# Optimization experiments

Measured on AMD Instinct MI355X. Metric: run time of the kernel, lower is better.

Reference implementation:

```python
import jax, jax.numpy as jnp
import numpy as np

N, E, P, IN, H = 1024, 65536, 1024, 128, 64
LN_EPS = 1e-5


def _layernorm(x, g, b):
    mu = x.mean(-1, keepdims=True)
    var = ((x - mu) ** 2).mean(-1, keepdims=True)
    return (x - mu) * jax.lax.rsqrt(var + LN_EPS) * g + b


def _gcn(x, ei, W, b, n):
    # PyG GCNConv: out = D^{-1/2} (A + I) D^{-1/2} X W + b
    row, col = ei[0], ei[1]
    xw = x @ W
    deg = jnp.zeros((n,), xw.dtype).at[col].add(1.0) + 1.0  # self-loop adds 1
    dinv = jax.lax.rsqrt(deg)
    coef = (dinv[row] * dinv[col])[:, None]
    out = jnp.zeros_like(xw).at[col].add(xw[row] * coef)
    out = out + xw * (dinv * dinv)[:, None]  # self-loop message
    return out + b


def setup_inputs() -> dict:
    key = jax.random.key(0)
    ks = jax.random.split(key, 20)
    f32 = jnp.float32
    inp = {
        "x": jax.random.normal(ks[0], (N, IN), f32),
        "ei": jax.random.randint(ks[1], (2, E), 0, N, dtype=jnp.int32),
        "pos": jax.random.randint(ks[2], (2, P), 0, N, dtype=jnp.int32),
        # GCNConv(input, hidden) and GCNConv(hidden, hidden)
        "W_g1": jax.random.normal(ks[3], (IN, H), f32) * (IN ** -0.5),
        "b_g1": jnp.zeros((H,), f32),
        "W_g2": jax.random.normal(ks[4], (H, H), f32) * (H ** -0.5),
        "b_g2": jnp.zeros((H,), f32),
        # mlp1: Linear + LayerNorm (+Dropout eval=id) + ReLU
        "W_m1": jax.random.normal(ks[5], (H, H), f32) * (H ** -0.5),
        "b_m1": jnp.zeros((H,), f32),
        "g_m1": jnp.ones((H,), f32),
        "be_m1": jnp.zeros((H,), f32),
        # mlp2
        "W_m2": jax.random.normal(ks[6], (H, H), f32) * (H ** -0.5),
        "b_m2": jnp.zeros((H,), f32),
        "g_m2": jnp.ones((H,), f32),
        "be_m2": jnp.zeros((H,), f32),
        # mlp3: Linear(2H,H) + ReLU + Linear(H,1)
        "W_a": jax.random.normal(ks[7], (2 * H, H), f32) * ((2 * H) ** -0.5),
        "b_a": jnp.zeros((H,), f32),
        "W_b": jax.random.normal(ks[8], (H, 1), f32) * (H ** -0.5),
        "b_b": jnp.zeros((1,), f32),
    }
    return inp


def reference(x, ei, pos, W_g1, b_g1, W_g2, b_g2, W_m1, b_m1, g_m1, be_m1,
              W_m2, b_m2, g_m2, be_m2, W_a, b_a, W_b, b_b):
    n = x.shape[0]
    # forward_routine
    h = _gcn(x, ei, W_g1, b_g1, n)
    h = _gcn(h, ei, W_g2, b_g2, n)
    xx = h[pos[0]] * h[pos[1]]          # [P, H] pairwise node products at queries
    xe = h[ei[0]] * h[ei[1]]            # [E, H] pairwise node products at edges
    x1 = jax.nn.relu(_layernorm(xe @ W_m1 + b_m1, g_m1, be_m1))  # mlp1
    x2 = jax.nn.relu(_layernorm(xe @ W_m2 + b_m2, g_m2, be_m2))  # mlp2
    # dense_bmm / sparse_bmm followed by combine() keeps only entries at pos
    # pairs, so compute res[pos0, pos1, :] = sum_k D1[pos0, k, :] * D2[k, pos1, :]
    D1 = jnp.zeros((n, n, H), x2.dtype).at[ei[0], ei[1]].set(x2)  # mlp2 output: left operand
    D2 = jnp.zeros((n, n, H), x1.dtype).at[ei[0], ei[1]].set(x1)  # mlp1 output: right operand
    r1 = D1[pos[0]]                                   # [P, N, H]
    c2 = jnp.swapaxes(jnp.take(D2, pos[1], axis=1), 0, 1)  # [P, N, H]
    pos_val = jnp.einsum('pnh,pnh->ph', r1, c2)       # [P, H]
    feat = jnp.concatenate([pos_val, xx], axis=1)     # combine -> [P, 2H]
    hid = jax.nn.relu(feat @ W_a + b_a)               # mlp3 (dropout = identity at eval)
    return (hid @ W_b + b_b).squeeze(-1)              # [P]
```

## Files before the change

kernel.cpp:

```cpp
#include <hip/hip_runtime.h>

#define Nn 1024
#define Ee 65536
#define Pq 1024
#define CAP 160

typedef unsigned long long ull;

__global__ __launch_bounds__(256) void k_zero(uint4* __restrict__ z) {
    z[blockIdx.x * 256 + threadIdx.x] = make_uint4(0, 0, 0, 0);
}

__global__ __launch_bounds__(256) void k_front(const float* __restrict__ x,
                                               const float* __restrict__ Wg1,
                                               float* __restrict__ xw1,
                                               const int* __restrict__ ei,
                                               int* __restrict__ degI,
                                               int* __restrict__ adj,
                                               ull* __restrict__ Mbit,
                                               ull* __restrict__ MTbit) {
    __shared__ float sW[8192];
    int tid = threadIdx.x;
    int B = blockIdx.x;
    if (B < 256) {
        int gid = B * 256 + tid;
        for (int i = tid; i < 2048; i += 256)
            ((float4*)sW)[i] = ((const float4*)Wg1)[i];
        __syncthreads();
        int lane = gid & 63;
        int r = __builtin_amdgcn_readfirstlane(gid >> 6);
        const float* xr = x + r * 128;
        float acc = 0.f;
        #pragma unroll 8
        for (int j = 0; j < 128; ++j) acc = fmaf(xr[j], sW[j * 64 + lane], acc);
        xw1[gid] = acc;
    } else {
        int e = (B - 256) * 256 + tid;
        int r = ei[e], c = ei[Ee + e];
        int slot = atomicAdd(&degI[c], 1);
        if (slot < CAP) adj[c * CAP + slot] = r;
        atomicOr(&Mbit[r * 16 + (c >> 6)], 1ull << (c & 63));
        atomicOr(&MTbit[c * 16 + (r >> 6)], 1ull << (r & 63));
    }
}

__device__ __forceinline__ float gather_quarter(const int* __restrict__ s_adj,
                                                const float* __restrict__ xwsrc,
                                                const float* s_dinv, int w,
                                                int n, int lane) {
    float acc = 0.f;
    int j = w, end = n;
    for (; j + 28 < end; j += 32) {
        int r0 = s_adj[j],      r1 = s_adj[j + 4],  r2 = s_adj[j + 8],  r3 = s_adj[j + 12];
        int r4 = s_adj[j + 16], r5 = s_adj[j + 20], r6 = s_adj[j + 24], r7 = s_adj[j + 28];
        float a0 = xwsrc[r0 * 64 + lane] * s_dinv[r0];
        float a1 = xwsrc[r1 * 64 + lane] * s_dinv[r1];
        float a2 = xwsrc[r2 * 64 + lane] * s_dinv[r2];
        float a3 = xwsrc[r3 * 64 + lane] * s_dinv[r3];
        float a4 = xwsrc[r4 * 64 + lane] * s_dinv[r4];
        float a5 = xwsrc[r5 * 64 + lane] * s_dinv[r5];
        float a6 = xwsrc[r6 * 64 + lane] * s_dinv[r6];
        float a7 = xwsrc[r7 * 64 + lane] * s_dinv[r7];
        acc += ((a0 + a1) + (a2 + a3)) + ((a4 + a5) + (a6 + a7));
    }
    for (; j < end; j += 4) {
        int r = s_adj[j];
        acc += xwsrc[r * 64 + lane] * s_dinv[r];
    }
    return acc;
}

__global__ __launch_bounds__(256) void k_gather1(const int* __restrict__ adj,
                                                 const int* __restrict__ degI,
                                                 const float* __restrict__ xw1,
                                                 const float* __restrict__ Wg2,
                                                 const float* __restrict__ bg1,
                                                 float* __restrict__ xw2) {
    __shared__ float sW[4096];
    __shared__ float s_dinv[Nn];
    __shared__ int s_adj[CAP];
    __shared__ float red[4][64];
    int tid = threadIdx.x;
    int lane = tid & 63;
    int w = tid >> 6;
    int c = blockIdx.x;
    for (int i = tid; i < 1024; i += 256)
        ((float4*)sW)[i] = ((const float4*)Wg2)[i];
    {
        int4 d4 = ((const int4*)degI)[tid];
        s_dinv[4 * tid]     = rsqrtf((float)d4.x + 1.f);
        s_dinv[4 * tid + 1] = rsqrtf((float)d4.y + 1.f);
        s_dinv[4 * tid + 2] = rsqrtf((float)d4.z + 1.f);
        s_dinv[4 * tid + 3] = rsqrtf((float)d4.w + 1.f);
    }
    int n = __builtin_amdgcn_readfirstlane(degI[c]);
    if (n > CAP) n = CAP;
    if (tid < n) s_adj[tid] = adj[c * CAP + tid];
    __syncthreads();
    float acc = gather_quarter(s_adj, xw1, s_dinv, w, n, lane);
    red[w][lane] = acc;
    __syncthreads();
    if (w == 0) {
        float a = (red[0][lane] + red[1][lane]) + (red[2][lane] + red[3][lane]);
        float dc = s_dinv[c];
        float h1c = dc * a + dc * dc * xw1[c * 64 + lane] + bg1[lane];
        float t = 0.f;
        #pragma unroll 8
        for (int j = 0; j < 64; ++j) t = fmaf(__shfl(h1c, j), sW[j * 64 + lane], t);
        xw2[c * 64 + lane] = t;
    }
}

__global__ __launch_bounds__(256) void k_gather2(const int* __restrict__ adj,
                                                 const int* __restrict__ degI,
                                                 const float* __restrict__ xw2,
                                                 const float* __restrict__ bg2,
                                                 float* __restrict__ h2) {
    __shared__ float s_dinv[Nn];
    __shared__ int s_adj[CAP];
    __shared__ float red[4][64];
    int tid = threadIdx.x;
    int lane = tid & 63;
    int w = tid >> 6;
    int c = blockIdx.x;
    {
        int4 d4 = ((const int4*)degI)[tid];
        s_dinv[4 * tid]     = rsqrtf((float)d4.x + 1.f);
        s_dinv[4 * tid + 1] = rsqrtf((float)d4.y + 1.f);
        s_dinv[4 * tid + 2] = rsqrtf((float)d4.z + 1.f);
        s_dinv[4 * tid + 3] = rsqrtf((float)d4.w + 1.f);
    }
    int n = __builtin_amdgcn_readfirstlane(degI[c]);
    if (n > CAP) n = CAP;
    if (tid < n) s_adj[tid] = adj[c * CAP + tid];
    __syncthreads();
    float acc = gather_quarter(s_adj, xw2, s_dinv, w, n, lane);
    red[w][lane] = acc;
    __syncthreads();
    if (w == 0) {
        float a = (red[0][lane] + red[1][lane]) + (red[2][lane] + red[3][lane]);
        float dc = s_dinv[c];
        h2[c * 64 + lane] = dc * a + dc * dc * xw2[c * 64 + lane] + bg2[lane];
    }
}

__global__ __launch_bounds__(256) void k_posfinal(
    const int* __restrict__ pos,
    const ull* __restrict__ Mbit, const ull* __restrict__ MTbit,
    const float* __restrict__ h2,
    const float* __restrict__ W1, const float* __restrict__ b1,
    const float* __restrict__ g1, const float* __restrict__ be1,
    const float* __restrict__ W2, const float* __restrict__ b2,
    const float* __restrict__ g2, const float* __restrict__ be2,
    const float* __restrict__ Wa, const float* __restrict__ ba,
    const float* __restrict__ Wb, const float* __restrict__ bb,
    float* __restrict__ out) {
    __shared__ float W1s[4096], W2s[4096];
    __shared__ float s_red[3][64];
    int tid = threadIdx.x;
    for (int i = tid; i < 1024; i += 256) {
        ((float4*)W1s)[i] = ((const float4*)W1)[i];
        ((float4*)W2s)[i] = ((const float4*)W2)[i];
    }
    __syncthreads();
    int lane = tid & 63;
    int wv = tid >> 6;
    int p = blockIdx.x;
    int a = __builtin_amdgcn_readfirstlane(pos[p]);
    int b = __builtin_amdgcn_readfirstlane(pos[Pq + p]);
    float ha = h2[a * 64 + lane], hb = h2[b * 64 + lane];
    float lb1 = b1[lane], lg1 = g1[lane], lbe1 = be1[lane];
    float lb2 = b2[lane], lg2 = g2[lane], lbe2 = be2[lane];
    float acc = 0.f;
    for (int wd = wv; wd < 16; wd += 4) {
        ull bits = Mbit[a * 16 + wd] & MTbit[b * 16 + wd];
        while (bits) {
            int k = (wd << 6) + __ffsll(bits) - 1;
            bits &= bits - 1;
            float hk = h2[k * 64 + lane];
            float xeA = ha * hk;
            float xeB = hk * hb;
            float a2 = lb2, a1 = lb1;
            #pragma unroll 8
            for (int j = 0; j < 64; ++j) {
                float vA = __shfl(xeA, j);
                float vB = __shfl(xeB, j);
                a2 = fmaf(vA, W2s[j * 64 + lane], a2);
                a1 = fmaf(vB, W1s[j * 64 + lane], a1);
            }
            float s2 = a2, q2 = a2 * a2, s1 = a1, q1 = a1 * a1;
            for (int off = 32; off; off >>= 1) {
                s2 += __shfl_xor(s2, off); q2 += __shfl_xor(q2, off);
                s1 += __shfl_xor(s1, off); q1 += __shfl_xor(q1, off);
            }
            float mu2 = s2 * (1.f / 64.f), mu1 = s1 * (1.f / 64.f);
            float v2 = q2 * (1.f / 64.f) - mu2 * mu2;
            float v1 = q1 * (1.f / 64.f) - mu1 * mu1;
            float r2v = rsqrtf(v2 + 1e-5f), r1v = rsqrtf(v1 + 1e-5f);
            float x2v = fmaxf(0.f, (a2 - mu2) * r2v * lg2 + lbe2);
            float x1v = fmaxf(0.f, (a1 - mu1) * r1v * lg1 + lbe1);
            acc += x2v * x1v;
        }
    }
    if (wv) s_red[wv - 1][lane] = acc;
    __syncthreads();
    if (wv == 0) {
        acc += (s_red[0][lane] + s_red[1][lane]) + s_red[2][lane];
        float xx = ha * hb;
        float t = ba[lane];
        #pragma unroll 8
        for (int j = 0; j < 64; ++j) {
            t = fmaf(__shfl(acc, j), Wa[j * 64 + lane], t);
            t = fmaf(__shfl(xx, j), Wa[(64 + j) * 64 + lane], t);
        }
        t = fmaxf(t, 0.f);
        float v = t * Wb[lane];
        for (int off = 32; off; off >>= 1) v += __shfl_xor(v, off);
        if (lane == 0) out[p] = v + bb[0];
    }
}

extern "C" void kernel_launch(void* const* d_in, const int* in_sizes, int n_in,
                              void* d_out, int out_size, void* d_ws, size_t ws_size,
                              hipStream_t stream) {
    const float* x    = (const float*)d_in[0];
    const int*   ei   = (const int*)d_in[1];
    const int*   pos  = (const int*)d_in[2];
    const float* Wg1  = (const float*)d_in[3];
    const float* bg1  = (const float*)d_in[4];
    const float* Wg2  = (const float*)d_in[5];
    const float* bg2  = (const float*)d_in[6];
    const float* Wm1  = (const float*)d_in[7];
    const float* bm1  = (const float*)d_in[8];
    const float* gm1  = (const float*)d_in[9];
    const float* bem1 = (const float*)d_in[10];
    const float* Wm2  = (const float*)d_in[11];
    const float* bm2  = (const float*)d_in[12];
    const float* gm2  = (const float*)d_in[13];
    const float* bem2 = (const float*)d_in[14];
    const float* Wa   = (const float*)d_in[15];
    const float* ba   = (const float*)d_in[16];
    const float* Wb   = (const float*)d_in[17];
    const float* bb   = (const float*)d_in[18];
    float* out = (float*)d_out;

    char* w = (char*)d_ws;
    char* zbase = w;
    int* degI = (int*)w;  w += 1024 * 4;
    ull* Mbit = (ull*)w;  w += 1024 * 16 * 8;
    ull* MTbit = (ull*)w; w += 1024 * 16 * 8;
    int*   adj = (int*)w;   w += (size_t)Nn * CAP * 4;
    float* xw1 = (float*)w; w += 65536 * 4;
    float* xw2 = (float*)w; w += 65536 * 4;
    float* h2  = (float*)w; w += 65536 * 4;

    k_zero<<<65, 256, 0, stream>>>((uint4*)zbase);
    k_front<<<512, 256, 0, stream>>>(x, Wg1, xw1, ei, degI, adj, Mbit, MTbit);
    k_gather1<<<Nn, 256, 0, stream>>>(adj, degI, xw1, Wg2, bg1, xw2);
    k_gather2<<<Nn, 256, 0, stream>>>(adj, degI, xw2, bg2, h2);
    k_posfinal<<<Pq, 256, 0, stream>>>(pos, Mbit, MTbit, h2,
                                       Wm1, bm1, gm1, bem1,
                                       Wm2, bm2, gm2, bem2,
                                       Wa, ba, Wb, bb, out);
}
```

Baseline: 63.77 us.

## Fuse second GCN gather into pair kernel, computing needed h2 rows on demand

Removes the separate k_gather2 launch and the h2 buffer. The pair kernel now recomputes the second-layer GCN aggregation only for the rows it needs (a, b and each common neighbour k). It also collects the hit list into shared memory first and spreads the hits over 8 waves in 512-thread blocks instead of scanning bitmask words per wave. This saves one launch and one global round trip. The cost is redundant per-hit gathers across blocks, and hit lists longer than 64 are silently truncated.

After: 66.13 us. 3.7% more time.

```diff
diff --git a/kernel.cpp b/kernel.cpp
--- a/kernel.cpp
+++ b/kernel.cpp
@@ -111,43 +111,43 @@
     }
 }
 
-__global__ __launch_bounds__(256) void k_gather2(const int* __restrict__ adj,
-                                                 const int* __restrict__ degI,
-                                                 const float* __restrict__ xw2,
-                                                 const float* __restrict__ bg2,
-                                                 float* __restrict__ h2) {
-    __shared__ float s_dinv[Nn];
-    __shared__ int s_adj[CAP];
-    __shared__ float red[4][64];
-    int tid = threadIdx.x;
-    int lane = tid & 63;
-    int w = tid >> 6;
-    int c = blockIdx.x;
-    {
-        int4 d4 = ((const int4*)degI)[tid];
-        s_dinv[4 * tid]     = rsqrtf((float)d4.x + 1.f);
-        s_dinv[4 * tid + 1] = rsqrtf((float)d4.y + 1.f);
-        s_dinv[4 * tid + 2] = rsqrtf((float)d4.z + 1.f);
-        s_dinv[4 * tid + 3] = rsqrtf((float)d4.w + 1.f);
-    }
-    int n = __builtin_amdgcn_readfirstlane(degI[c]);
+__device__ __forceinline__ float row_h2(const int* __restrict__ adj,
+                                        const int* __restrict__ degI,
+                                        const float* __restrict__ xw2,
+                                        const float* s_dinv,
+                                        const float* __restrict__ bg2,
+                                        int r, int lane) {
+    const int* al = adj + r * CAP;
+    int n = __builtin_amdgcn_readfirstlane(degI[r]);
     if (n > CAP) n = CAP;
-    if (tid < n) s_adj[tid] = adj[c * CAP + tid];
-    __syncthreads();
-    float acc = gather_quarter(s_adj, xw2, s_dinv, w, n, lane);
-    red[w][lane] = acc;
-    __syncthreads();
-    if (w == 0) {
-        float a = (red[0][lane] + red[1][lane]) + (red[2][lane] + red[3][lane]);
-        float dc = s_dinv[c];
-        h2[c * 64 + lane] = dc * a + dc * dc * xw2[c * 64 + lane] + bg2[lane];
-    }
-}
-
-__global__ __launch_bounds__(256) void k_posfinal(
+    float acc = 0.f;
+    int j = 0;
+    for (; j + 7 < n; j += 8) {
+        int r0 = al[j],     r1 = al[j + 1], r2 = al[j + 2], r3 = al[j + 3];
+        int r4 = al[j + 4], r5 = al[j + 5], r6 = al[j + 6], r7 = al[j + 7];
+        float a0 = xw2[r0 * 64 + lane] * s_dinv[r0];
+        float a1 = xw2[r1 * 64 + lane] * s_dinv[r1];
+        float a2 = xw2[r2 * 64 + lane] * s_dinv[r2];
+        float a3 = xw2[r3 * 64 + lane] * s_dinv[r3];
+        float a4 = xw2[r4 * 64 + lane] * s_dinv[r4];
+        float a5 = xw2[r5 * 64 + lane] * s_dinv[r5];
+        float a6 = xw2[r6 * 64 + lane] * s_dinv[r6];
+        float a7 = xw2[r7 * 64 + lane] * s_dinv[r7];
+        acc += ((a0 + a1) + (a2 + a3)) + ((a4 + a5) + (a6 + a7));
+    }
+    for (; j < n; ++j) {
+        int rr = al[j];
+        acc += xw2[rr * 64 + lane] * s_dinv[rr];
+    }
+    float dr = s_dinv[r];
+    return dr * acc + dr * dr * xw2[r * 64 + lane] + bg2[lane];
+}
+
+__global__ __launch_bounds__(512) void k_posfinal2(
     const int* __restrict__ pos,
     const ull* __restrict__ Mbit, const ull* __restrict__ MTbit,
-    const float* __restrict__ h2,
+    const int* __restrict__ adj, const int* __restrict__ degI,
+    const float* __restrict__ xw2, const float* __restrict__ bg2,
     const float* __restrict__ W1, const float* __restrict__ b1,
     const float* __restrict__ g1, const float* __restrict__ be1,
     const float* __restrict__ W2, const float* __restrict__ b2,
@@ -156,61 +156,87 @@
     const float* __restrict__ Wb, const float* __restrict__ bb,
     float* __restrict__ out) {
     __shared__ float W1s[4096], W2s[4096];
-    __shared__ float s_red[3][64];
+    __shared__ float s_dinv[Nn];
+    __shared__ float s_ha[64], s_hb[64];
+    __shared__ float s_red[8][64];
+    __shared__ int s_hits[64];
+    __shared__ int s_nhit;
     int tid = threadIdx.x;
-    for (int i = tid; i < 1024; i += 256) {
+    int lane = tid & 63;
+    int wv = tid >> 6;
+    if (tid == 0) s_nhit = 0;
+    for (int i = tid; i < 1024; i += 512) {
         ((float4*)W1s)[i] = ((const float4*)W1)[i];
         ((float4*)W2s)[i] = ((const float4*)W2)[i];
     }
-    __syncthreads();
-    int lane = tid & 63;
-    int wv = tid >> 6;
+    {
+        int2 d2 = ((const int2*)degI)[tid];
+        s_dinv[2 * tid]     = rsqrtf((float)d2.x + 1.f);
+        s_dinv[2 * tid + 1] = rsqrtf((float)d2.y + 1.f);
+    }
     int p = blockIdx.x;
     int a = __builtin_amdgcn_readfirstlane(pos[p]);
     int b = __builtin_amdgcn_readfirstlane(pos[Pq + p]);
-    float ha = h2[a * 64 + lane], hb = h2[b * 64 + lane];
+    __syncthreads();
+
+    if (wv == 0) {
+        s_ha[lane] = row_h2(adj, degI, xw2, s_dinv, bg2, a, lane);
+    } else if (wv == 1) {
+        s_hb[lane] = row_h2(adj, degI, xw2, s_dinv, bg2, b, lane);
+    } else if (wv == 2 && lane < 16) {
+        ull bits = Mbit[a * 16 + lane] & MTbit[b * 16 + lane];
+        while (bits) {
+            int k = (lane << 6) + __ffsll(bits) - 1;
+            bits &= bits - 1;
+            int idx = atomicAdd(&s_nhit, 1);
+            if (idx < 64) s_hits[idx] = k;
+        }
+    }
+    __syncthreads();
+
+    int nh = s_nhit;
+    if (nh > 64) nh = 64;
+    float ha = s_ha[lane], hb = s_hb[lane];
     float lb1 = b1[lane], lg1 = g1[lane], lbe1 = be1[lane];
     float lb2 = b2[lane], lg2 = g2[lane], lbe2 = be2[lane];
     float acc = 0.f;
-    for (int wd = wv; wd < 16; wd += 4) {
-        ull bits = Mbit[a * 16 + wd] & MTbit[b * 16 + wd];
-        while (bits) {
-            int k = (wd << 6) + __ffsll(bits) - 1;
-            bits &= bits - 1;
-            float hk = h2[k * 64 + lane];
-            float xeA = ha * hk;
-            float xeB = hk * hb;
-            float a2 = lb2, a1 = lb1;
-            #pragma unroll 8
-            for (int j = 0; j < 64; ++j) {
-                float vA = __shfl(xeA, j);
-                float vB = __shfl(xeB, j);
-                a2 = fmaf(vA, W2s[j * 64 + lane], a2);
-                a1 = fmaf(vB, W1s[j * 64 + lane], a1);
-            }
-            float s2 = a2, q2 = a2 * a2, s1 = a1, q1 = a1 * a1;
-            for (int off = 32; off; off >>= 1) {
-                s2 += __shfl_xor(s2, off); q2 += __shfl_xor(q2, off);
-                s1 += __shfl_xor(s1, off); q1 += __shfl_xor(q1, off);
-            }
-            float mu2 = s2 * (1.f / 64.f), mu1 = s1 * (1.f / 64.f);
-            float v2 = q2 * (1.f / 64.f) - mu2 * mu2;
-            float v1 = q1 * (1.f / 64.f) - mu1 * mu1;
-            float r2v = rsqrtf(v2 + 1e-5f), r1v = rsqrtf(v1 + 1e-5f);
-            float x2v = fmaxf(0.f, (a2 - mu2) * r2v * lg2 + lbe2);
-            float x1v = fmaxf(0.f, (a1 - mu1) * r1v * lg1 + lbe1);
-            acc += x2v * x1v;
-        }
-    }
-    if (wv) s_red[wv - 1][lane] = acc;
+    for (int i = wv; i < nh; i += 8) {
+        int k = __builtin_amdgcn_readfirstlane(s_hits[i]);
+        float hk = row_h2(adj, degI, xw2, s_dinv, bg2, k, lane);
+        float xeA = ha * hk;
+        float xeB = hk * hb;
+        float a2 = lb2, a1 = lb1;
+        #pragma unroll 8
+        for (int j = 0; j < 64; ++j) {
+            float vA = __shfl(xeA, j);
+            float vB = __shfl(xeB, j);
+            a2 = fmaf(vA, W2s[j * 64 + lane], a2);
+            a1 = fmaf(vB, W1s[j * 64 + lane], a1);
+        }
+        float s2 = a2, q2 = a2 * a2, s1 = a1, q1 = a1 * a1;
+        for (int off = 32; off; off >>= 1) {
+            s2 += __shfl_xor(s2, off); q2 += __shfl_xor(q2, off);
+            s1 += __shfl_xor(s1, off); q1 += __shfl_xor(q1, off);
+        }
+        float mu2 = s2 * (1.f / 64.f), mu1 = s1 * (1.f / 64.f);
+        float v2 = q2 * (1.f / 64.f) - mu2 * mu2;
+        float v1 = q1 * (1.f / 64.f) - mu1 * mu1;
+        float r2v = rsqrtf(v2 + 1e-5f), r1v = rsqrtf(v1 + 1e-5f);
+        float x2v = fmaxf(0.f, (a2 - mu2) * r2v * lg2 + lbe2);
+        float x1v = fmaxf(0.f, (a1 - mu1) * r1v * lg1 + lbe1);
+        acc += x2v * x1v;
+    }
+    s_red[wv][lane] = acc;
     __syncthreads();
     if (wv == 0) {
-        acc += (s_red[0][lane] + s_red[1][lane]) + s_red[2][lane];
+        float A = 0.f;
+        #pragma unroll
+        for (int w2i = 0; w2i < 8; ++w2i) A += s_red[w2i][lane];
         float xx = ha * hb;
         float t = ba[lane];
         #pragma unroll 8
         for (int j = 0; j < 64; ++j) {
-            t = fmaf(__shfl(acc, j), Wa[j * 64 + lane], t);
+            t = fmaf(__shfl(A, j), Wa[j * 64 + lane], t);
             t = fmaf(__shfl(xx, j), Wa[(64 + j) * 64 + lane], t);
         }
         t = fmaxf(t, 0.f);
@@ -252,14 +278,12 @@
     int*   adj = (int*)w;   w += (size_t)Nn * CAP * 4;
     float* xw1 = (float*)w; w += 65536 * 4;
     float* xw2 = (float*)w; w += 65536 * 4;
-    float* h2  = (float*)w; w += 65536 * 4;
 
     k_zero<<<65, 256, 0, stream>>>((uint4*)zbase);
     k_front<<<512, 256, 0, stream>>>(x, Wg1, xw1, ei, degI, adj, Mbit, MTbit);
     k_gather1<<<Nn, 256, 0, stream>>>(adj, degI, xw1, Wg2, bg1, xw2);
-    k_gather2<<<Nn, 256, 0, stream>>>(adj, degI, xw2, bg2, h2);
-    k_posfinal<<<Pq, 256, 0, stream>>>(pos, Mbit, MTbit, h2,
-                                       Wm1, bm1, gm1, bem1,
-                                       Wm2, bm2, gm2, bem2,
-                                       Wa, ba, Wb, bb, out);
-}
+    k_posfinal2<<<Pq, 512, 0, stream>>>(pos, Mbit, MTbit, adj, degI, xw2, bg2,
+                                        Wm1, bm1, gm1, bem1,
+                                        Wm2, bm2, gm2, bem2,
+                                        Wa, ba, Wb, bb, out);
+}
```
